# Kernel tuning notes

Hardware: AMD Instinct MI355X
Metric: run time of the kernel (lower is better)

Reference implementation:

```python
import jax, jax.numpy as jnp
import numpy as np

N_NODES = 100000
N_EDGES = 3200000
F_IN = 128
F_OUT = 16


def setup_inputs() -> dict:
    key = jax.random.key(0)
    k1, k2, k3, k4, k5 = jax.random.split(key, 5)
    x = jax.random.normal(k1, (N_NODES, F_IN), dtype=jnp.float32)
    edge_index = jax.random.randint(k2, (2, N_EDGES), 0, N_NODES, dtype=jnp.int64)
    edge_weights = jax.random.uniform(k3, (N_EDGES,), dtype=jnp.float32)
    W = jax.random.normal(k4, (F_IN, F_OUT), dtype=jnp.float32) / np.sqrt(F_IN)
    b = jax.random.normal(k5, (F_OUT,), dtype=jnp.float32)
    return {"x": x, "edge_index": edge_index, "edge_weights": edge_weights, "W": W, "b": b}


def reference(x, edge_index, edge_weights, W, b):
    # GCNConv: out = D^{-1/2} (A + I) D^{-1/2} X W + b  (weighted edges, self-loops)
    n = x.shape[0]
    row = edge_index[0]  # source nodes
    col = edge_index[1]  # target nodes (aggregation destination)
    # add self-loops with weight 1.0 (GCNConv default)
    loop = jnp.arange(n, dtype=row.dtype)
    row_f = jnp.concatenate([row, loop])
    col_f = jnp.concatenate([col, loop])
    ew = jnp.concatenate([edge_weights, jnp.ones((n,), dtype=edge_weights.dtype)])
    # symmetric normalization: deg over destination, norm = d^{-1/2}[row] * w * d^{-1/2}[col]
    deg = jax.ops.segment_sum(ew, col_f, num_segments=n)
    dinv = jnp.where(deg > 0, jax.lax.rsqrt(deg), 0.0)
    norm = dinv[row_f] * ew * dinv[col_f]  # [E+N]
    h = x @ W  # [N, F_OUT] dense projection before propagation
    msgs = h[row_f] * norm[:, None]  # gather + scale, [E+N, F_OUT]
    out = jax.ops.segment_sum(msgs, col_f, num_segments=n)  # scatter-add
    return out + b
```

## Files before the change

kernel.cpp:

```cpp
#include <hip/hip_runtime.h>

#define N_NODES 100000
#define N_EDGES 3200000
#define F_IN 128
#define F_OUT 16

#define NSEG 1024
#define EPS (N_EDGES / NSEG)
#define EPT 7
#define NBUCK 512
#define NPB 196
#define CAPR 7424
#define RPT 29
#define CURSTRIDE 16
#define GEMM32 ((N_NODES + 31) / 32)
#define PULL_BLOCKS 2048

#define OFF_CUR   0x000000u
#define OFF_NPTR  0x010000u
#define OFF_NCNT  0x080000u
#define OFF_DINV  0x0F0000u
#define OFF_HH    0x160000u
#define OFF_GG    0x780000u
#define OFF_CSR   0xB00000u
#define WS_NEEDED ((size_t)0x1000000 + (size_t)N_EDGES * 8)

__device__ __forceinline__ unsigned short f2bf(float f) {
    unsigned u = __float_as_uint(f);
    unsigned r = (u + 0x7FFFu + ((u >> 16) & 1u)) >> 16;
    return (unsigned short)r;
}
__device__ __forceinline__ float bf2f(unsigned short v) {
    return __uint_as_float((unsigned)v << 16);
}


__global__ void __launch_bounds__(512, 4) k_binC(const int* __restrict__ row,
                                                 const int* __restrict__ col,
                                                 const float* __restrict__ ew,
                                                 int* __restrict__ cursor,
                                                 int2* __restrict__ csr,
                                                 const float* __restrict__ x,
                                                 const float* __restrict__ W,
                                                 float* __restrict__ h) {
    __shared__ int2 srec[EPS];
    __shared__ unsigned char sbk[EPS];
    __shared__ int lcnt[NBUCK];
    __shared__ int lpre[NBUCK];
    __shared__ int gofs[NBUCK];
    __shared__ int wtot[8];
    int tid = threadIdx.x;
    if (blockIdx.x < NSEG) {
        int e0 = blockIdx.x * EPS;
        lcnt[tid] = 0;
        __syncthreads();

        int2 rec[EPT];
        int meta[EPT];
#pragma unroll
        for (int k = 0; k < EPT; ++k) {
            int i = k * 512 + tid;
            if (k < EPT - 1 || i < EPS) {
                int e = e0 + i;
                int r = row[e];
                int c = col[e];
                float w = ew[e];
                int bk = c / NPB;
                int pos = atomicAdd(&lcnt[bk], 1);
                rec[k] = make_int2((r << 8) | (c - bk * NPB), __float_as_int(w));
                meta[k] = (bk << 16) | pos;
            }
        }
        __syncthreads();

        int v = lcnt[tid];
        int inc = v;
#pragma unroll
        for (int off = 1; off < 64; off <<= 1) {
            int t = __shfl_up(inc, off);
            if ((tid & 63) >= off) inc += t;
        }
        if ((tid & 63) == 63) wtot[tid >> 6] = inc;
        __syncthreads();
        int woff = 0;
#pragma unroll
        for (int k = 0; k < 8; ++k)
            if (k < (tid >> 6)) woff += wtot[k];
        int excl = woff + inc - v;
        lpre[tid] = excl;
        gofs[tid] = tid * CAPR + atomicAdd(&cursor[tid * CURSTRIDE], v) - excl;
        __syncthreads();

        int mid = lpre[256];
#pragma unroll
        for (int k = 0; k < EPT; ++k) {
            int i = k * 512 + tid;
            if (k < EPT - 1 || i < EPS) {
                int m = meta[k];
                int slot = lpre[m >> 16] + (m & 0xFFFF);
                srec[slot] = rec[k];
                sbk[slot] = (unsigned char)(m >> 16);
            }
        }
        __syncthreads();

        for (int t = tid; t < EPS; t += 512) {
            int bk = sbk[t] + ((t >= mid) ? 256 : 0);
            csr[gofs[bk] + t] = srec[t];
        }
    } else {
        float* Ws = (float*)srec;
        for (int i = tid; i < F_IN * F_OUT; i += 512) Ws[i] = W[i];
        __syncthreads();
        int n = (blockIdx.x - NSEG) * 32 + (tid >> 4);
        int j = tid & 15;
        if (n >= N_NODES) return;
        const float4* xr = (const float4*)(x + (size_t)n * F_IN);
        float acc = 0.0f;
#pragma unroll
        for (int k4 = 0; k4 < F_IN / 4; ++k4) {
            float4 xv = xr[k4];
            int k = k4 * 4;
            acc += xv.x * Ws[(k + 0) * F_OUT + j];
            acc += xv.y * Ws[(k + 1) * F_OUT + j];
            acc += xv.z * Ws[(k + 2) * F_OUT + j];
            acc += xv.w * Ws[(k + 3) * F_OUT + j];
        }
        h[(size_t)n * F_OUT + j] = acc;
    }
}

__global__ void __launch_bounds__(256, 4) k_sortB(const int* __restrict__ cursor,
                                                  int2* __restrict__ csr,
                                                  const float* __restrict__ h,
                                                  float* __restrict__ dinv,
                                                  unsigned short* __restrict__ gb,
                                                  int* __restrict__ nodeptr,
                                                  int* __restrict__ ncnt) {
    __shared__ int cnt[256];
    __shared__ int basel[256];
    __shared__ int wtot[4];
    __shared__ float dl[256];
    int tid = threadIdx.x;
    int b = blockIdx.x;
    int c0 = b * NPB;
    int rb = b * CAPR;
    int total = cursor[b * CURSTRIDE];
    if (total > CAPR) total = CAPR;

    cnt[tid] = 0;
    __syncthreads();

    int2 rec[RPT];
    int pos[RPT];
#pragma unroll
    for (int k = 0; k < RPT; ++k) {
        int i = k * 256 + tid;
        if (i < total) {
            rec[k] = csr[rb + i];
            pos[k] = atomicAdd(&cnt[rec[k].x & 255], 1);
        }
    }
    __syncthreads();

    int v = cnt[tid];
    int inc = v;
#pragma unroll
    for (int off = 1; off < 64; off <<= 1) {
        int t = __shfl_up(inc, off);
        if ((tid & 63) >= off) inc += t;
    }
    if ((tid & 63) == 63) wtot[tid >> 6] = inc;
    __syncthreads();
    int woff = 0;
#pragma unroll
    for (int k = 0; k < 4; ++k)
        if (k < (tid >> 6)) woff += wtot[k];
    int excl = woff + inc - v;
    int n = c0 + tid;
    if (tid < NPB && n < N_NODES) {
        nodeptr[n] = rb + excl;
        ncnt[n] = v;
    }
    basel[tid] = excl;
    __syncthreads();

#pragma unroll
    for (int k = 0; k < RPT; ++k) {
        int i = k * 256 + tid;
        if (i < total) {
            int cl = rec[k].x & 255;
            csr[rb + basel[cl] + pos[k]] = make_int2(rec[k].x >> 8, rec[k].y);
        }
    }
    __syncthreads();

    float d = 0.0f;
    if (tid < NPB && n < N_NODES) {
        float s = 1.0f;
        const int2* run = csr + rb + excl;
        for (int k = 0; k < v; ++k) s += __int_as_float(run[k].y);
        d = rsqrtf(s);
        dinv[n] = d;
    }
    dl[tid] = d;
    __syncthreads();
    for (int i = tid; i < NPB * F_OUT; i += 256) {
        int idx = c0 * F_OUT + i;
        if (idx < N_NODES * F_OUT) gb[idx] = f2bf(dl[i >> 4] * h[idx]);
    }
}

__global__ void __launch_bounds__(256) k_pull4(const int* __restrict__ nodeptr,
                                               const int* __restrict__ ncnt,
                                               const int2* __restrict__ csr,
                                               const unsigned short* __restrict__ gb,
                                               const float* __restrict__ dinv,
                                               const float* __restrict__ bias,
                                               float* __restrict__ out) {
    int wid = threadIdx.x >> 6;
    int lane = threadIdx.x & 63;
    int l4 = lane & 15;
    int fr = ((l4 & 1) << 3) | ((l4 & 2) << 1) | ((l4 & 4) >> 1) | ((l4 & 8) >> 3);
    float bj = bias[fr];
    for (int n = blockIdx.x * 4 + wid; n < N_NODES; n += PULL_BLOCKS * 4) {
        int p0 = nodeptr[n];
        int c = ncnt[n];
        float acc[16];
#pragma unroll
        for (int k = 0; k < 16; ++k) acc[k] = 0.0f;
        for (int base = 0; base < c; base += 64) {
            int i = base + lane;
            int2 rec = (i < c) ? csr[p0 + i] : make_int2(0, 0);
            float w = __int_as_float(rec.y);
            const uint4* gr = (const uint4*)(gb + ((size_t)rec.x << 4));
            uint4 qa = gr[0];
            uint4 qb = gr[1];
            acc[0]  += w * __uint_as_float(qa.x << 16);
            acc[1]  += w * __uint_as_float(qa.x & 0xFFFF0000u);
            acc[2]  += w * __uint_as_float(qa.y << 16);
            acc[3]  += w * __uint_as_float(qa.y & 0xFFFF0000u);
            acc[4]  += w * __uint_as_float(qa.z << 16);
            acc[5]  += w * __uint_as_float(qa.z & 0xFFFF0000u);
            acc[6]  += w * __uint_as_float(qa.w << 16);
            acc[7]  += w * __uint_as_float(qa.w & 0xFFFF0000u);
            acc[8]  += w * __uint_as_float(qb.x << 16);
            acc[9]  += w * __uint_as_float(qb.x & 0xFFFF0000u);
            acc[10] += w * __uint_as_float(qb.y << 16);
            acc[11] += w * __uint_as_float(qb.y & 0xFFFF0000u);
            acc[12] += w * __uint_as_float(qb.z << 16);
            acc[13] += w * __uint_as_float(qb.z & 0xFFFF0000u);
            acc[14] += w * __uint_as_float(qb.w << 16);
            acc[15] += w * __uint_as_float(qb.w & 0xFFFF0000u);
        }
        bool b1 = (lane & 1) != 0;
#pragma unroll
        for (int k = 0; k < 8; ++k) {
            float keep = b1 ? acc[k + 8] : acc[k];
            float send = b1 ? acc[k] : acc[k + 8];
            acc[k] = keep + __shfl_xor(send, 1);
        }
        bool b2 = (lane & 2) != 0;
#pragma unroll
        for (int k = 0; k < 4; ++k) {
            float keep = b2 ? acc[k + 4] : acc[k];
            float send = b2 ? acc[k] : acc[k + 4];
            acc[k] = keep + __shfl_xor(send, 2);
        }
        bool b4 = (lane & 4) != 0;
#pragma unroll
        for (int k = 0; k < 2; ++k) {
            float keep = b4 ? acc[k + 2] : acc[k];
            float send = b4 ? acc[k] : acc[k + 2];
            acc[k] = keep + __shfl_xor(send, 4);
        }
        bool b8 = (lane & 8) != 0;
        {
            float keep = b8 ? acc[1] : acc[0];
            float send = b8 ? acc[0] : acc[1];
            acc[0] = keep + __shfl_xor(send, 8);
        }
        acc[0] += __shfl_xor(acc[0], 16);
        acc[0] += __shfl_xor(acc[0], 32);
        if (lane < 16) {
            float d = dinv[n];
            float gs = bf2f(gb[(size_t)n * F_OUT + fr]);
            out[(size_t)n * F_OUT + fr] = bj + d * (gs + acc[0]);
        }
    }
}


#define EDGE_BLOCKS_FB ((N_EDGES + 255) / 256)
#define GEMM_BLOCKS_FB ((N_NODES + 15) / 16)
__global__ void k_init_fb(float* __restrict__ deg) {
    int i = blockIdx.x * blockDim.x + threadIdx.x;
    if (i < N_NODES) deg[i] = 1.0f;
}
__global__ void k_fused_fb(const int* __restrict__ col, const float* __restrict__ ew,
                           float* __restrict__ deg, const float* __restrict__ x,
                           const float* __restrict__ W, float* __restrict__ h) {
    int b3 = blockIdx.x / 3;
    int r3 = blockIdx.x % 3;
    if (r3 < 2) {
        int e = (b3 * 2 + r3) * 256 + threadIdx.x;
        if (e < N_EDGES) atomicAdd(&deg[col[e]], ew[e]);
    } else {
        __shared__ float Ws[F_IN * F_OUT];
        int tid = threadIdx.x;
        for (int i = tid; i < F_IN * F_OUT; i += 256) Ws[i] = W[i];
        __syncthreads();
        int n = b3 * 16 + (tid >> 4);
        int j = tid & 15;
        if (n >= N_NODES) return;
        const float4* xr = (const float4*)(x + (size_t)n * F_IN);
        float acc = 0.0f;
#pragma unroll
        for (int k4 = 0; k4 < F_IN / 4; ++k4) {
            float4 xv = xr[k4];
            int k = k4 * 4;
            acc += xv.x * Ws[(k + 0) * F_OUT + j];
            acc += xv.y * Ws[(k + 1) * F_OUT + j];
            acc += xv.z * Ws[(k + 2) * F_OUT + j];
            acc += xv.w * Ws[(k + 3) * F_OUT + j];
        }
        h[(size_t)n * F_OUT + j] = acc;
    }
}
__global__ void k_final_fb(float* __restrict__ deg, const float* __restrict__ h,
                           const float* __restrict__ b, float* __restrict__ g,
                           float* __restrict__ out) {
    int i = blockIdx.x * blockDim.x + threadIdx.x;
    int n = i >> 4;
    int j = i & 15;
    if (n >= N_NODES) return;
    float d = rsqrtf(deg[n]);
    if (j == 0) deg[n] = d;
    float gg = d * h[i];
    g[i] = gg;
    out[i] = b[j] + d * gg;
}
__global__ void k_scatter_fb(const int* __restrict__ row, const int* __restrict__ col,
                             const float* __restrict__ ew, const float* __restrict__ dinv,
                             const float* __restrict__ g, float* __restrict__ out) {
    long long tid = (long long)blockIdx.x * blockDim.x + threadIdx.x;
    int e = (int)(tid >> 4);
    int j = (int)(tid & 15);
    if (e >= N_EDGES) return;
    int c = col[e];
    float norm = ew[e] * dinv[c];
    atomicAdd(&out[(size_t)c * F_OUT + j], g[(size_t)row[e] * F_OUT + j] * norm);
}

extern "C" void kernel_launch(void* const* d_in, const int* in_sizes, int n_in,
                              void* d_out, int out_size, void* d_ws, size_t ws_size,
                              hipStream_t stream) {
    const float* x  = (const float*)d_in[0];
    const int*   ei = (const int*)d_in[1];
    const float* ew = (const float*)d_in[2];
    const float* W  = (const float*)d_in[3];
    const float* b  = (const float*)d_in[4];
    float* out = (float*)d_out;

    const int* row = ei;
    const int* col = ei + N_EDGES;

    char* ws = (char*)d_ws;
    dim3 blk(256);

    if (ws_size >= WS_NEEDED) {
        int*   cur  = (int*)(ws + OFF_CUR);
        int*   nptr = (int*)(ws + OFF_NPTR);
        int*   ncnt = (int*)(ws + OFF_NCNT);
        float* dinv = (float*)(ws + OFF_DINV);
        float* h    = (float*)(ws + OFF_HH);
        unsigned short* gb = (unsigned short*)(ws + OFF_GG);
        int2*  csr  = (int2*)(ws + OFF_CSR);

        hipMemsetAsync(cur, 0, NBUCK * CURSTRIDE * sizeof(int), stream);
        k_binC<<<NSEG + GEMM32, 512, 0, stream>>>(row, col, ew, cur, csr, x, W, h);
        k_sortB<<<NBUCK, blk, 0, stream>>>(cur, csr, h, dinv, gb, nptr, ncnt);
        k_pull4<<<PULL_BLOCKS, blk, 0, stream>>>(nptr, ncnt, csr, gb, dinv, b, out);
    } else {
        float* deg = (float*)ws;
        float* h   = (float*)(ws + (1u << 20));
        float* g   = (float*)(ws + (8u << 20));
        k_init_fb<<<(N_NODES + 255) / 256, blk, 0, stream>>>(deg);
        k_fused_fb<<<EDGE_BLOCKS_FB + GEMM_BLOCKS_FB, blk, 0, stream>>>(col, ew, deg, x, W, h);
        k_final_fb<<<(N_NODES * F_OUT + 255) / 256, blk, 0, stream>>>(deg, h, b, g, out);
        long long total = (long long)N_EDGES * F_OUT;
        k_scatter_fb<<<(unsigned)((total + 255) / 256), blk, 0, stream>>>(row, col, ew, deg, g, out);
    }
}
```

Measured before the change: 246.7 us.

## Fuse bucket sort with pull aggregation in LDS, compute degrees via atomics

Degree sums are now accumulated during binning with fixed-point integer atomics, and a small prep kernel computes dinv and the bf16-scaled features. The second-level sort no longer writes back to global memory. Each bucket block keeps its records and a permutation in LDS and aggregates directly per node, 16 lanes per feature and 4 edge slices. Buckets grow from 512 to 768 so each block's records fit in shared memory. The cost is extra global atomics per edge, a fixed-point degree that only approximates the float sum, and narrower 2-byte gathers.

Result: slower. 388.2 us (+57.4%).

```diff
diff --git a/kernel.cpp b/kernel.cpp
--- a/kernel.cpp
+++ b/kernel.cpp
@@ -8,20 +8,18 @@
 #define NSEG 1024
 #define EPS (N_EDGES / NSEG)
 #define EPT 7
-#define NBUCK 512
-#define NPB 196
-#define CAPR 7424
-#define RPT 29
+#define NBUCK 768
+#define NPB 131
+#define CAPR 4944
+#define RPT 20
 #define CURSTRIDE 16
 #define GEMM32 ((N_NODES + 31) / 32)
-#define PULL_BLOCKS 2048
 
 #define OFF_CUR   0x000000u
-#define OFF_NPTR  0x010000u
-#define OFF_NCNT  0x080000u
-#define OFF_DINV  0x0F0000u
-#define OFF_HH    0x160000u
-#define OFF_GG    0x780000u
+#define OFF_WSI   0x010000u
+#define OFF_DINV  0x090000u
+#define OFF_HH    0x100000u
+#define OFF_GG    0x720000u
 #define OFF_CSR   0xB00000u
 #define WS_NEEDED ((size_t)0x1000000 + (size_t)N_EDGES * 8)
 
@@ -35,14 +33,15 @@
 }
 
 
-__global__ void __launch_bounds__(512, 4) k_binC(const int* __restrict__ row,
-                                                 const int* __restrict__ col,
-                                                 const float* __restrict__ ew,
-                                                 int* __restrict__ cursor,
-                                                 int2* __restrict__ csr,
-                                                 const float* __restrict__ x,
-                                                 const float* __restrict__ W,
-                                                 float* __restrict__ h) {
+__global__ void __launch_bounds__(512) k_binD(const int* __restrict__ row,
+                                              const int* __restrict__ col,
+                                              const float* __restrict__ ew,
+                                              int* __restrict__ cursor,
+                                              int* __restrict__ wsum_i,
+                                              int2* __restrict__ csr,
+                                              const float* __restrict__ x,
+                                              const float* __restrict__ W,
+                                              float* __restrict__ h) {
     __shared__ int2 srec[EPS];
     __shared__ unsigned char sbk[EPS];
     __shared__ int lcnt[NBUCK];
@@ -52,7 +51,7 @@
     int tid = threadIdx.x;
     if (blockIdx.x < NSEG) {
         int e0 = blockIdx.x * EPS;
-        lcnt[tid] = 0;
+        for (int i = tid; i < NBUCK; i += 512) lcnt[i] = 0;
         __syncthreads();
 
         int2 rec[EPT];
@@ -67,31 +66,43 @@
                 float w = ew[e];
                 int bk = c / NPB;
                 int pos = atomicAdd(&lcnt[bk], 1);
+                atomicAdd(&wsum_i[c], __float2int_rn(w * 1048576.0f));
                 rec[k] = make_int2((r << 8) | (c - bk * NPB), __float_as_int(w));
                 meta[k] = (bk << 16) | pos;
             }
         }
         __syncthreads();
 
-        int v = lcnt[tid];
-        int inc = v;
+        int v0 = 0, v1 = 0, ssum = 0;
+        if (tid < 384) {
+            v0 = lcnt[2 * tid];
+            v1 = lcnt[2 * tid + 1];
+            ssum = v0 + v1;
+        }
+        int inc = ssum;
 #pragma unroll
         for (int off = 1; off < 64; off <<= 1) {
             int t = __shfl_up(inc, off);
             if ((tid & 63) >= off) inc += t;
         }
-        if ((tid & 63) == 63) wtot[tid >> 6] = inc;
-        __syncthreads();
-        int woff = 0;
-#pragma unroll
-        for (int k = 0; k < 8; ++k)
-            if (k < (tid >> 6)) woff += wtot[k];
-        int excl = woff + inc - v;
-        lpre[tid] = excl;
-        gofs[tid] = tid * CAPR + atomicAdd(&cursor[tid * CURSTRIDE], v) - excl;
-        __syncthreads();
-
-        int mid = lpre[256];
+        if ((tid & 63) == 63 && tid < 384) wtot[tid >> 6] = inc;
+        __syncthreads();
+        if (tid < 384) {
+            int woff = 0;
+#pragma unroll
+            for (int k = 0; k < 6; ++k)
+                if (k < (tid >> 6)) woff += wtot[k];
+            int excl = woff + inc - ssum;
+            lpre[2 * tid] = excl;
+            lpre[2 * tid + 1] = excl + v0;
+            int b0 = 2 * tid, b1 = 2 * tid + 1;
+            gofs[b0] = b0 * CAPR + atomicAdd(&cursor[b0 * CURSTRIDE], v0) - excl;
+            gofs[b1] = b1 * CAPR + atomicAdd(&cursor[b1 * CURSTRIDE], v1) - (excl + v0);
+        }
+        __syncthreads();
+
+        int mid1 = lpre[256];
+        int mid2 = lpre[512];
 #pragma unroll
         for (int k = 0; k < EPT; ++k) {
             int i = k * 512 + tid;
@@ -105,7 +116,7 @@
         __syncthreads();
 
         for (int t = tid; t < EPS; t += 512) {
-            int bk = sbk[t] + ((t >= mid) ? 256 : 0);
+            int bk = sbk[t] + ((t >= mid2) ? 512 : ((t >= mid1) ? 256 : 0));
             csr[gofs[bk] + t] = srec[t];
         }
     } else {
@@ -130,17 +141,31 @@
     }
 }
 
-__global__ void __launch_bounds__(256, 4) k_sortB(const int* __restrict__ cursor,
-                                                  int2* __restrict__ csr,
-                                                  const float* __restrict__ h,
-                                                  float* __restrict__ dinv,
-                                                  unsigned short* __restrict__ gb,
-                                                  int* __restrict__ nodeptr,
-                                                  int* __restrict__ ncnt) {
+__global__ void k_prep(const int* __restrict__ wsum_i, const float* __restrict__ h,
+                       float* __restrict__ dinv, unsigned short* __restrict__ gb) {
+    int t = blockIdx.x * 256 + threadIdx.x;
+    if (t >= N_NODES * 4) return;
+    int n = t >> 2;
+    float d = rsqrtf(1.0f + (float)wsum_i[n] * (1.0f / 1048576.0f));
+    if ((t & 3) == 0) dinv[n] = d;
+    float4 hv = ((const float4*)h)[t];
+    unsigned o0 = (unsigned)f2bf(d * hv.x) | ((unsigned)f2bf(d * hv.y) << 16);
+    unsigned o1 = (unsigned)f2bf(d * hv.z) | ((unsigned)f2bf(d * hv.w) << 16);
+    uint2 o; o.x = o0; o.y = o1;
+    ((uint2*)gb)[t] = o;
+}
+
+__global__ void __launch_bounds__(256, 3) k_bpull(const int* __restrict__ cursor,
+                                                  const int2* __restrict__ csr,
+                                                  const unsigned short* __restrict__ gb,
+                                                  const float* __restrict__ dinv,
+                                                  const float* __restrict__ bias,
+                                                  float* __restrict__ out) {
+    __shared__ int2 srec[CAPR];
+    __shared__ unsigned short perm[CAPR];
     __shared__ int cnt[256];
     __shared__ int basel[256];
     __shared__ int wtot[4];
-    __shared__ float dl[256];
     int tid = threadIdx.x;
     int b = blockIdx.x;
     int c0 = b * NPB;
@@ -151,14 +176,15 @@
     cnt[tid] = 0;
     __syncthreads();
 
-    int2 rec[RPT];
-    int pos[RPT];
+    int meta[RPT];
 #pragma unroll
     for (int k = 0; k < RPT; ++k) {
         int i = k * 256 + tid;
         if (i < total) {
-            rec[k] = csr[rb + i];
-            pos[k] = atomicAdd(&cnt[rec[k].x & 255], 1);
+            int2 rec = csr[rb + i];
+            srec[i] = rec;
+            int cl = rec.x & 255;
+            meta[k] = (cl << 16) | atomicAdd(&cnt[cl], 1);
         }
     }
     __syncthreads();
@@ -176,116 +202,41 @@
 #pragma unroll
     for (int k = 0; k < 4; ++k)
         if (k < (tid >> 6)) woff += wtot[k];
-    int excl = woff + inc - v;
-    int n = c0 + tid;
-    if (tid < NPB && n < N_NODES) {
-        nodeptr[n] = rb + excl;
-        ncnt[n] = v;
-    }
-    basel[tid] = excl;
+    basel[tid] = woff + inc - v;
     __syncthreads();
 
 #pragma unroll
     for (int k = 0; k < RPT; ++k) {
         int i = k * 256 + tid;
         if (i < total) {
-            int cl = rec[k].x & 255;
-            csr[rb + basel[cl] + pos[k]] = make_int2(rec[k].x >> 8, rec[k].y);
-        }
-    }
-    __syncthreads();
-
-    float d = 0.0f;
-    if (tid < NPB && n < N_NODES) {
-        float s = 1.0f;
-        const int2* run = csr + rb + excl;
-        for (int k = 0; k < v; ++k) s += __int_as_float(run[k].y);
-        d = rsqrtf(s);
-        dinv[n] = d;
-    }
-    dl[tid] = d;
-    __syncthreads();
-    for (int i = tid; i < NPB * F_OUT; i += 256) {
-        int idx = c0 * F_OUT + i;
-        if (idx < N_NODES * F_OUT) gb[idx] = f2bf(dl[i >> 4] * h[idx]);
-    }
-}
-
-__global__ void __launch_bounds__(256) k_pull4(const int* __restrict__ nodeptr,
-                                               const int* __restrict__ ncnt,
-                                               const int2* __restrict__ csr,
-                                               const unsigned short* __restrict__ gb,
-                                               const float* __restrict__ dinv,
-                                               const float* __restrict__ bias,
-                                               float* __restrict__ out) {
-    int wid = threadIdx.x >> 6;
-    int lane = threadIdx.x & 63;
-    int l4 = lane & 15;
-    int fr = ((l4 & 1) << 3) | ((l4 & 2) << 1) | ((l4 & 4) >> 1) | ((l4 & 8) >> 3);
-    float bj = bias[fr];
-    for (int n = blockIdx.x * 4 + wid; n < N_NODES; n += PULL_BLOCKS * 4) {
-        int p0 = nodeptr[n];
-        int c = ncnt[n];
-        float acc[16];
-#pragma unroll
-        for (int k = 0; k < 16; ++k) acc[k] = 0.0f;
-        for (int base = 0; base < c; base += 64) {
-            int i = base + lane;
-            int2 rec = (i < c) ? csr[p0 + i] : make_int2(0, 0);
-            float w = __int_as_float(rec.y);
-            const uint4* gr = (const uint4*)(gb + ((size_t)rec.x << 4));
-            uint4 qa = gr[0];
-            uint4 qb = gr[1];
-            acc[0]  += w * __uint_as_float(qa.x << 16);
-            acc[1]  += w * __uint_as_float(qa.x & 0xFFFF0000u);
-            acc[2]  += w * __uint_as_float(qa.y << 16);
-            acc[3]  += w * __uint_as_float(qa.y & 0xFFFF0000u);
-            acc[4]  += w * __uint_as_float(qa.z << 16);
-            acc[5]  += w * __uint_as_float(qa.z & 0xFFFF0000u);
-            acc[6]  += w * __uint_as_float(qa.w << 16);
-            acc[7]  += w * __uint_as_float(qa.w & 0xFFFF0000u);
-            acc[8]  += w * __uint_as_float(qb.x << 16);
-            acc[9]  += w * __uint_as_float(qb.x & 0xFFFF0000u);
-            acc[10] += w * __uint_as_float(qb.y << 16);
-            acc[11] += w * __uint_as_float(qb.y & 0xFFFF0000u);
-            acc[12] += w * __uint_as_float(qb.z << 16);
-            acc[13] += w * __uint_as_float(qb.z & 0xFFFF0000u);
-            acc[14] += w * __uint_as_float(qb.w << 16);
-            acc[15] += w * __uint_as_float(qb.w & 0xFFFF0000u);
-        }
-        bool b1 = (lane & 1) != 0;
-#pragma unroll
-        for (int k = 0; k < 8; ++k) {
-            float keep = b1 ? acc[k + 8] : acc[k];
-            float send = b1 ? acc[k] : acc[k + 8];
-            acc[k] = keep + __shfl_xor(send, 1);
-        }
-        bool b2 = (lane & 2) != 0;
-#pragma unroll
-        for (int k = 0; k < 4; ++k) {
-            float keep = b2 ? acc[k + 4] : acc[k];
-            float send = b2 ? acc[k] : acc[k + 4];
-            acc[k] = keep + __shfl_xor(send, 2);
-        }
-        bool b4 = (lane & 4) != 0;
-#pragma unroll
-        for (int k = 0; k < 2; ++k) {
-            float keep = b4 ? acc[k + 2] : acc[k];
-            float send = b4 ? acc[k] : acc[k + 2];
-            acc[k] = keep + __shfl_xor(send, 4);
-        }
-        bool b8 = (lane & 8) != 0;
-        {
-            float keep = b8 ? acc[1] : acc[0];
-            float send = b8 ? acc[0] : acc[1];
-            acc[0] = keep + __shfl_xor(send, 8);
-        }
-        acc[0] += __shfl_xor(acc[0], 16);
-        acc[0] += __shfl_xor(acc[0], 32);
-        if (lane < 16) {
+            int m = meta[k];
+            perm[basel[m >> 16] + (m & 0xFFFF)] = (unsigned short)i;
+        }
+    }
+    __syncthreads();
+
+    int wv = tid >> 6;
+    int lane = tid & 63;
+    int s = lane >> 4;
+    int j = lane & 15;
+    float bj = bias[j];
+    for (int nn = wv; nn < NPB; nn += 4) {
+        int n = c0 + nn;
+        if (n >= N_NODES) break;
+        int cv = cnt[nn];
+        int base = basel[nn];
+        float acc = 0.0f;
+        for (int i = s; i < cv; i += 4) {
+            int idx = perm[base + i];
+            int2 rc = srec[idx];
+            acc += __int_as_float(rc.y) * bf2f(gb[(size_t)(rc.x >> 8) * F_OUT + j]);
+        }
+        acc += __shfl_xor(acc, 16);
+        acc += __shfl_xor(acc, 32);
+        if (s == 0) {
             float d = dinv[n];
-            float gs = bf2f(gb[(size_t)n * F_OUT + fr]);
-            out[(size_t)n * F_OUT + fr] = bj + d * (gs + acc[0]);
+            float gs = bf2f(gb[(size_t)n * F_OUT + j]);
+            out[(size_t)n * F_OUT + j] = bj + d * (gs + acc);
         }
     }
 }
@@ -370,17 +321,16 @@
 
     if (ws_size >= WS_NEEDED) {
         int*   cur  = (int*)(ws + OFF_CUR);
-        int*   nptr = (int*)(ws + OFF_NPTR);
-        int*   ncnt = (int*)(ws + OFF_NCNT);
+        int*   wsi  = (int*)(ws + OFF_WSI);
         float* dinv = (float*)(ws + OFF_DINV);
         float* h    = (float*)(ws + OFF_HH);
         unsigned short* gb = (unsigned short*)(ws + OFF_GG);
         int2*  csr  = (int2*)(ws + OFF_CSR);
 
-        hipMemsetAsync(cur, 0, NBUCK * CURSTRIDE * sizeof(int), stream);
-        k_binC<<<NSEG + GEMM32, 512, 0, stream>>>(row, col, ew, cur, csr, x, W, h);
-        k_sortB<<<NBUCK, blk, 0, stream>>>(cur, csr, h, dinv, gb, nptr, ncnt);
-        k_pull4<<<PULL_BLOCKS, blk, 0, stream>>>(nptr, ncnt, csr, gb, dinv, b, out);
+        hipMemsetAsync(ws, 0, 0x90000, stream);
+        k_binD<<<NSEG + GEMM32, 512, 0, stream>>>(row, col, ew, cur, wsi, csr, x, W, h);
+        k_prep<<<(N_NODES * 4 + 255) / 256, blk, 0, stream>>>(wsi, h, dinv, gb);
+        k_bpull<<<NBUCK, blk, 0, stream>>>(cur, csr, gb, dinv, b, out);
     } else {
         float* deg = (float*)ws;
         float* h   = (float*)(ws + (1u << 20));
```
